# Performance work log

Hardware: AMD Instinct MI355X
Metric: run time of the kernel (lower is better)

Reference implementation:

```python
import jax, jax.numpy as jnp
import numpy as np

B, S, E, H, NE, TOPK = 8, 1024, 768, 12, 8, 2
F = 4 * E
DH = E // H

def _ln(x, g, b, eps=1e-5):
    m = jnp.mean(x, axis=-1, keepdims=True)
    v = jnp.mean((x - m) ** 2, axis=-1, keepdims=True)
    return (x - m) / jnp.sqrt(v + eps) * g + b

def _expert(x, lg, lb, w1, b1, w2, b2):
    # Expert: LayerNorm -> Linear(E,4E) -> GELU(exact) -> Linear(4E,E); dropout is identity in eval
    h = _ln(x, lg, lb)
    h = jax.nn.gelu(h @ w1.T + b1, approximate=False)
    return h @ w2.T + b2

def setup_inputs():
    key = jax.random.key(0)
    ks = jax.random.split(key, 16)
    rn = lambda k, shape, s=0.02: jax.random.normal(k, shape, jnp.float32) * s
    return {
        'x': jax.random.normal(ks[0], (B, S, E), jnp.float32),
        'modality_type': jax.random.randint(ks[1], (B, S), 0, 2).astype(jnp.int32),
        'norm1_g': jnp.ones((E,), jnp.float32), 'norm1_b': jnp.zeros((E,), jnp.float32),
        'norm2_g': jnp.ones((E,), jnp.float32), 'norm2_b': jnp.zeros((E,), jnp.float32),
        'in_proj_w': rn(ks[2], (3 * E, E)), 'in_proj_b': jnp.zeros((3 * E,), jnp.float32),
        'out_proj_w': rn(ks[3], (E, E)), 'out_proj_b': jnp.zeros((E,), jnp.float32),
        'router_w': rn(ks[4], (NE, E)), 'router_b': jnp.zeros((NE,), jnp.float32),
        'spec_ln_g': jnp.ones((3, E), jnp.float32), 'spec_ln_b': jnp.zeros((3, E), jnp.float32),
        'spec_w1': rn(ks[5], (3, F, E)), 'spec_b1': jnp.zeros((3, F), jnp.float32),
        'spec_w2': rn(ks[6], (3, E, F)), 'spec_b2': jnp.zeros((3, E), jnp.float32),
        'gen_ln_g': jnp.ones((NE, E), jnp.float32), 'gen_ln_b': jnp.zeros((NE, E), jnp.float32),
        'gen_w1': rn(ks[7], (NE, F, E)), 'gen_b1': jnp.zeros((NE, F), jnp.float32),
        'gen_w2': rn(ks[8], (NE, E, F)), 'gen_b2': jnp.zeros((NE, E), jnp.float32),
    }

def _forward(x, modality_type, norm1_g, norm1_b, norm2_g, norm2_b, in_proj_w, in_proj_b,
             out_proj_w, out_proj_b, router_w, router_b,
             spec_ln_g, spec_ln_b, spec_w1, spec_b1, spec_w2, spec_b2,
             gen_ln_g, gen_ln_b, gen_w1, gen_b1, gen_w2, gen_b2):
    # --- self-attention block (pre-norm + residual), matches nn.MultiheadAttention ---
    residual = x
    xn = _ln(x, norm1_g, norm1_b)
    qkv = xn @ in_proj_w.T + in_proj_b                          # [B,S,3E]
    q, k, v = jnp.split(qkv, 3, axis=-1)
    q = q.reshape(B, S, H, DH); k = k.reshape(B, S, H, DH); v = v.reshape(B, S, H, DH)
    scores = jnp.einsum('bqhd,bkhd->bhqk', q, k) / jnp.sqrt(jnp.float32(DH))
    attn = jax.nn.softmax(scores, axis=-1)
    ctx = jnp.einsum('bhqk,bkhd->bqhd', attn, v).reshape(B, S, E)
    x = residual + (ctx @ out_proj_w.T + out_proj_b)

    # --- MoE block (pre-norm + residual) ---
    residual = x
    xn = _ln(x, norm2_g, norm2_b)
    expert_out = _expert(xn, spec_ln_g[0], spec_ln_b[0], spec_w1[0], spec_b1[0], spec_w2[0], spec_b2[0])
    # modality experts: vision on tokens with type==0, text on type==1 (not a fusion layer)
    vmask = (modality_type == 0).astype(xn.dtype)[..., None]
    tmask = (modality_type == 1).astype(xn.dtype)[..., None]
    expert_out = expert_out + vmask * _expert(xn, spec_ln_g[1], spec_ln_b[1], spec_w1[1], spec_b1[1], spec_w2[1], spec_b2[1])
    expert_out = expert_out + tmask * _expert(xn, spec_ln_g[2], spec_ln_b[2], spec_w1[2], spec_b1[2], spec_w2[2], spec_b2[2])

    # --- router: softmax -> top_k -> renormalize over top_k ---
    logits = xn @ router_w.T + router_b                         # [B,S,NE]
    probs = jax.nn.softmax(logits, axis=-1)
    topk_probs, topk_idx = jax.lax.top_k(probs, TOPK)
    topk_w = jax.nn.softmax(topk_probs, axis=-1)                # [B,S,TOPK]

    # --- dispatch/combine: per-expert combine coefficient; experts are per-token so
    # dense masked compute is mathematically identical to the torch gather/scatter loop ---
    for e in range(NE):
        coef = jnp.sum(topk_w * (topk_idx == e), axis=-1)[..., None]   # [B,S,1]
        expert_out = expert_out + coef * _expert(xn, gen_ln_g[e], gen_ln_b[e], gen_w1[e], gen_b1[e], gen_w2[e], gen_b2[e])

    return residual + expert_out

def reference(x, modality_type, norm1_g, norm1_b, norm2_g, norm2_b, in_proj_w, in_proj_b,
              out_proj_w, out_proj_b, router_w, router_b,
              spec_ln_g, spec_ln_b, spec_w1, spec_b1, spec_w2, spec_b2,
              gen_ln_g, gen_ln_b, gen_w1, gen_b1, gen_w2, gen_b2):
    return _forward(x, modality_type, norm1_g, norm1_b, norm2_g, norm2_b, in_proj_w, in_proj_b,
                    out_proj_w, out_proj_b, router_w, router_b,
                    spec_ln_g, spec_ln_b, spec_w1, spec_b1, spec_w2, spec_b2,
                    gen_ln_g, gen_ln_b, gen_w1, gen_b1, gen_w2, gen_b2)
```

## Files before the change

kernel.cpp:

```cpp
#include <hip/hip_runtime.h>
#include <cstdint>

#define NTOK 8192
#define EDIM 768
#define FDIM 3072

using bf16x8 = __attribute__((ext_vector_type(8))) __bf16;
using f32x4  = __attribute__((ext_vector_type(4))) float;

__device__ __forceinline__ float b2f(ushort u){ union{uint32_t i; float f;} v; v.i = ((uint32_t)u)<<16; return v.f; }
__device__ __forceinline__ ushort f2b(float f){ union{float f; uint32_t i;} v; v.f=f; uint32_t r = v.i + 0x7fffu + ((v.i>>16)&1u); return (ushort)(r>>16); }
__device__ __forceinline__ float gelu_f(float v){
  float c = v*(1.5957691216f + 0.0713548162726f*v*v);
  return v / (1.f + __expf(-c));
}
__device__ __forceinline__ void gload16(const ushort* g, ushort* l){
  __builtin_amdgcn_global_load_lds((const __attribute__((address_space(1))) void*)g,
                                   (__attribute__((address_space(3))) void*)l, 16, 0, 0);
}

__global__ __launch_bounds__(256) void conv_w(const float* w0,const float* w1,const float* w2,
                                              const float* w3,const float* w4,const float* w5,
                                              const float* slg, const float* glg,
                                              ushort* pool)
{
  size_t idx4 = (size_t)blockIdx.x*256 + threadIdx.x;
  size_t e = idx4*4;
  const float* src; size_t base; int region;
  if      (e <  1769472u){src=w0;base=0;        region=0;}
  else if (e <  2359296u){src=w1;base=1769472u; region=1;}
  else if (e <  9437184u){src=w2;base=2359296u; region=2;}
  else if (e < 16515072u){src=w3;base=9437184u; region=3;}
  else if (e < 35389440u){src=w4;base=16515072u;region=4;}
  else                   {src=w5;base=35389440u;region=5;}
  size_t within = e - base;
  f32x4 f = *(const f32x4*)(src + within);
  if (region==2){
    int ex = (int)(within/2359296u); int col = (int)(within%768u);
    f32x4 g = *(const f32x4*)(slg + ex*768 + col);
    f[0]*=g[0]; f[1]*=g[1]; f[2]*=g[2]; f[3]*=g[3];
  } else if (region==4){
    int ex = (int)(within/2359296u); int col = (int)(within%768u);
    f32x4 g = *(const f32x4*)(glg + ex*768 + col);
    f[0]*=g[0]; f[1]*=g[1]; f[2]*=g[2]; f[3]*=g[3];
  }
  ushort4 u; u.x=f2b(f[0]); u.y=f2b(f[1]); u.z=f2b(f[2]); u.w=f2b(f[3]);
  *(ushort4*)(pool+e) = u;
}

__global__ __launch_bounds__(256) void b1fold_k(const float* __restrict__ sw1, const float* __restrict__ gw1,
                                                const float* __restrict__ sb1, const float* __restrict__ gb1,
                                                const float* __restrict__ slb, const float* __restrict__ glb,
                                                float* __restrict__ b1p)
{
  int j = blockIdx.x*4 + (threadIdx.x>>6);
  int lane = threadIdx.x & 63;
  int je = j / FDIM, f = j % FDIM;
  const float* wrow = (je<3) ? sw1 + ((size_t)je*FDIM + f)*EDIM : gw1 + ((size_t)(je-3)*FDIM + f)*EDIM;
  const float* lb   = (je<3) ? slb + (size_t)je*EDIM : glb + (size_t)(je-3)*EDIM;
  float s = 0.f;
  #pragma unroll
  for (int i=0;i<12;i++){ int d = lane + 64*i; s += wrow[d]*lb[d]; }
  #pragma unroll
  for (int o=32;o>0;o>>=1) s += __shfl_xor(s,o);
  if (lane==0){
    float base = (je<3) ? sb1[je*FDIM+f] : gb1[(je-3)*FDIM+f];
    b1p[j] = base + s;
  }
}

__global__ __launch_bounds__(256) void out_init(const float* __restrict__ x, const float* __restrict__ bo,
                                                float* __restrict__ out)
{
  size_t i = ((size_t)blockIdx.x*256 + threadIdx.x)*4;
  int col = (int)(i % EDIM);
  f32x4 xv = *(const f32x4*)(x+i);
  f32x4 bv = *(const f32x4*)(bo+col);
  f32x4 r = { xv[0]+bv[0], xv[1]+bv[1], xv[2]+bv[2], xv[3]+bv[3] };
  *(f32x4*)(out+i) = r;
}

__global__ __launch_bounds__(256) void ln1_k(const float* __restrict__ x, const float* __restrict__ g,
                                             const float* __restrict__ b, ushort* __restrict__ out)
{
  int w = blockIdx.x*4 + (threadIdx.x>>6);
  int lane = threadIdx.x & 63;
  const float* xr = x + (size_t)w*EDIM;
  float v[12]; float s=0.f, s2=0.f;
  #pragma unroll
  for (int i=0;i<12;i++){ v[i]=xr[lane+64*i]; s+=v[i]; s2+=v[i]*v[i]; }
  #pragma unroll
  for (int o=32;o>0;o>>=1){ s += __shfl_xor(s,o); s2 += __shfl_xor(s2,o); }
  float mu = s*(1.f/768.f);
  float rs = rsqrtf(s2*(1.f/768.f) - mu*mu + 1e-5f);
  ushort* op = out + (size_t)w*EDIM;
  #pragma unroll
  for (int i=0;i<12;i++){ int d=lane+64*i; op[d] = f2b((v[i]-mu)*rs*g[d] + b[d]); }
}

__global__ __launch_bounds__(256) void lnr_k(const float* __restrict__ x1, const float* __restrict__ g2,
                                             const float* __restrict__ b2, const float* __restrict__ rw,
                                             const float* __restrict__ rbv,
                                             ushort* __restrict__ z, float* __restrict__ coef)
{
  int w = blockIdx.x*4 + (threadIdx.x>>6);
  int lane = threadIdx.x & 63;
  const float* xr = x1 + (size_t)w*EDIM;
  float v[12]; float s=0.f, s2=0.f;
  #pragma unroll
  for (int i=0;i<12;i++){ v[i]=xr[lane+64*i]; s+=v[i]; s2+=v[i]*v[i]; }
  #pragma unroll
  for (int o=32;o>0;o>>=1){ s += __shfl_xor(s,o); s2 += __shfl_xor(s2,o); }
  float mu = s*(1.f/768.f);
  float rs = rsqrtf(s2*(1.f/768.f) - mu*mu + 1e-5f);
  float xn[12]; s=0.f; s2=0.f;
  #pragma unroll
  for (int i=0;i<12;i++){ int d=lane+64*i; xn[i]=(v[i]-mu)*rs*g2[d]+b2[d]; s+=xn[i]; s2+=xn[i]*xn[i]; }
  float pl[8] = {0.f,0.f,0.f,0.f,0.f,0.f,0.f,0.f};
  #pragma unroll
  for (int i=0;i<12;i++){
    int d=lane+64*i; float xv=xn[i];
    #pragma unroll
    for (int e=0;e<8;e++) pl[e] += xv * rw[e*EDIM + d];
  }
  #pragma unroll
  for (int o=32;o>0;o>>=1){ s += __shfl_xor(s,o); s2 += __shfl_xor(s2,o); }
  float mu2 = s*(1.f/768.f);
  float rs2 = rsqrtf(s2*(1.f/768.f) - mu2*mu2 + 1e-5f);
  ushort* op = z + (size_t)w*EDIM;
  #pragma unroll
  for (int i=0;i<12;i++){ int d=lane+64*i; op[d] = f2b((xn[i]-mu2)*rs2); }
  #pragma unroll
  for (int e=0;e<8;e++){
    #pragma unroll
    for (int o=32;o>0;o>>=1) pl[e] += __shfl_xor(pl[e], o);
  }
  float lgt[8]; float mx = -1e30f;
  #pragma unroll
  for (int e=0;e<8;e++){ lgt[e]=pl[e]+rbv[e]; mx = fmaxf(mx, lgt[e]); }
  float p[8]; float den=0.f;
  #pragma unroll
  for (int e=0;e<8;e++){ p[e]=__expf(lgt[e]-mx); den+=p[e]; }
  float inv = 1.f/den;
  #pragma unroll
  for (int e=0;e<8;e++) p[e]*=inv;
  int i1=0;
  #pragma unroll
  for (int e=1;e<8;e++) if (p[e]>p[i1]) i1=e;
  int i2=(i1==0)?1:0;
  #pragma unroll
  for (int e=0;e<8;e++){ if (e==i1) continue; if (p[e]>p[i2]) i2=e; }
  float w1 = 1.f/(1.f+__expf(p[i2]-p[i1]));
  float w2 = 1.f - w1;
  if (lane < 8){
    float c = (lane==i1)? w1 : ((lane==i2)? w2 : 0.f);
    coef[(size_t)w*8 + lane] = c;
  }
}

__global__ __launch_bounds__(256) void build_lists(const int* __restrict__ mt, const float* __restrict__ coef,
                                                   ushort* __restrict__ lists, ushort* __restrict__ inv,
                                                   int* __restrict__ cnt)
{
  const int job = blockIdx.x;
  ushort* list = lists + (size_t)job*NTOK;
  __shared__ int wsum[4];
  int base = 0;
  const int lane = threadIdx.x & 63, wv = threadIdx.x >> 6;
  for (int c0=0; c0<NTOK; c0+=256){
    int t = c0 + threadIdx.x;
    bool flag;
    if (job==0)      flag = (mt[t]==0);
    else if (job==1) flag = (mt[t]==1);
    else             flag = (coef[(size_t)t*8 + (job-2)] != 0.0f);
    unsigned long long bal = __ballot(flag);
    int pre = __popcll(bal & ((1ull<<lane)-1ull));
    if (lane==0) wsum[wv] = __popcll(bal);
    __syncthreads();
    int off = base + pre;
    for (int k=0;k<wv;k++) off += wsum[k];
    int tot = wsum[0]+wsum[1]+wsum[2]+wsum[3];
    if (flag){ list[off] = (ushort)t; inv[(size_t)job*NTOK + t] = (ushort)off; }
    base += tot;
    __syncthreads();
  }
  if (threadIdx.x==0){ cnt[job+1] = base; if (job==0) cnt[0] = NTOK; }
}

__global__ __launch_bounds__(256) void gather_k(const float* __restrict__ coef, const int* __restrict__ mt,
                                                const ushort* __restrict__ inv, const int* __restrict__ cnt,
                                                const ushort* __restrict__ outC, float* __restrict__ out,
                                                int phase)
{
  int t = blockIdx.x*4 + (threadIdx.x>>6);
  int lane = threadIdx.x & 63;
  int r0, r1; float c0=1.f, c1=1.f;
  if (phase==0){
    r0 = t;
    int m = mt[t];
    r1 = NTOK + (m ? cnt[1] : 0) + (int)inv[(size_t)m*NTOK + t];
  } else {
    int found=0; int rr[2]={0,0}; float cc[2]={0.f,0.f}; int base=0;
    #pragma unroll
    for (int e=0;e<8;e++){
      float ce = coef[(size_t)t*8+e];
      if (ce != 0.f && found<2){ rr[found]=base+(int)inv[(size_t)(2+e)*NTOK + t]; cc[found]=ce; found++; }
      base += cnt[3+e];
    }
    r0=rr[0]; r1=rr[1]; c0=cc[0]; c1=cc[1];
  }
  const ushort* pa = outC + (size_t)r0*EDIM;
  const ushort* pb = outC + (size_t)r1*EDIM;
  float* po = out + (size_t)t*EDIM;
  #pragma unroll
  for (int i=0;i<3;i++){
    int d = lane*4 + 256*i;
    ushort4 ua = *(const ushort4*)(pa+d);
    ushort4 ub = *(const ushort4*)(pb+d);
    f32x4 o = *(f32x4*)(po+d);
    o[0] += c0*b2f(ua.x) + c1*b2f(ub.x);
    o[1] += c0*b2f(ua.y) + c1*b2f(ub.y);
    o[2] += c0*b2f(ua.z) + c1*b2f(ub.z);
    o[3] += c0*b2f(ua.w) + c1*b2f(ub.w);
    *(f32x4*)(po+d) = o;
  }
}

struct GemmArgs {
  const ushort* A; const ushort* B;
  const float* bias;
  ushort* outBF;
  int K, ldc;
};

__global__ __launch_bounds__(256) void gemm_k(GemmArgs g)
{
  const int mb = blockIdx.x, nb = blockIdx.y;
  __shared__ __align__(1024) ushort As[128*32];
  __shared__ __align__(1024) ushort Bs[128*32];
  const int tid = threadIdx.x;
  const int lane = tid & 63, w = tid >> 6;
  const int seg = lane & 3;
  const int lrow = w*16 + (lane>>2);
  const int p = (lane>>3)&3;
  ushort* ldsA0 = As + (size_t)w*512;
  ushort* ldsA1 = As + (size_t)(w+4)*512;
  ushort* ldsB0 = Bs + (size_t)w*512;
  ushort* ldsB1 = Bs + (size_t)(w+4)*512;
  const int KK = g.K;
  const ushort* pA0 = g.A + (size_t)(mb*128 + lrow)*KK + (seg^p)*8;
  const ushort* pA1 = pA0 + (size_t)64*KK;
  const ushort* pB0 = g.B + (size_t)(nb*128 + lrow)*KK + (seg^p)*8;
  const ushort* pB1 = pB0 + (size_t)64*KK;
  const int nst = KK >> 5;
  f32x4 acc[4][4];
  #pragma unroll
  for (int m=0;m<4;m++)
    #pragma unroll
    for (int n=0;n<4;n++) acc[m][n] = (f32x4){0.f,0.f,0.f,0.f};
  const int fr = lane & 15, fq = lane >> 4;
  const int pr = (fr>>1)&3;
  const int so = (fq^pr)*8;
  const int rb_ = (w>>1)*64, cb_ = (w&1)*64;
  for (int kt=0; kt<nst; ++kt){
    __syncthreads();
    gload16(pA0, ldsA0); gload16(pA1, ldsA1);
    gload16(pB0, ldsB0); gload16(pB1, ldsB1);
    pA0 += 32; pA1 += 32; pB0 += 32; pB1 += 32;
    __syncthreads();
    bf16x8 af[4], bfr[4];
    #pragma unroll
    for (int m=0;m<4;m++) af[m]  = *(const bf16x8*)&As[(rb_ + m*16 + fr)*32 + so];
    #pragma unroll
    for (int n=0;n<4;n++) bfr[n] = *(const bf16x8*)&Bs[(cb_ + n*16 + fr)*32 + so];
    #pragma unroll
    for (int m=0;m<4;m++)
      #pragma unroll
      for (int n=0;n<4;n++)
        acc[m][n] = __builtin_amdgcn_mfma_f32_16x16x32_bf16(af[m], bfr[n], acc[m][n], 0, 0, 0);
  }
  #pragma unroll
  for (int m=0;m<4;m++){
    #pragma unroll
    for (int j=0;j<4;j++){
      const int row = mb*128 + rb_ + m*16 + fq*4 + j;
      #pragma unroll
      for (int n=0;n<4;n++){
        const int col = nb*128 + cb_ + n*16 + fr;
        g.outBF[(size_t)row*g.ldc + col] = f2b(acc[m][n][j] + g.bias[col]);
      }
    }
  }
}

struct FArgs {
  const ushort* z; ushort* hidden; const ushort* ctx; const ushort* wo;
  float* out; ushort* outC;
  const ushort* lists; const ushort* inv; const int* cnt; const float* coef;
  const ushort* sw1; const ushort* gw1; const ushort* sw2; const ushort* gw2;
  const float* b1p; const float* sb2; const float* gb2;
  int jobBase; int compact; int mode;
};

__device__ __forceinline__ size_t job_hoff(const FArgs& a, int job){
  size_t h = 0;
  if (a.compact){
    if (job==1) h = NTOK;
    else if (job==2) h = NTOK + (size_t)a.cnt[1];
    else if (job>=3){ for (int k=3;k<job;k++) h += (size_t)a.cnt[k]; }
  }
  return h;
}

__global__ __launch_bounds__(512) void ffn1_k(FArgs a)
{
  const int job = a.jobBase + blockIdx.z;
  const int cntj = (job==0) ? NTOK : a.cnt[job];
  const int mb = blockIdx.x, nb = blockIdx.y;
  if (mb*128 >= cntj) return;
  const ushort* list = (job==0) ? nullptr : a.lists + (size_t)(job-1)*NTOK;
  const ushort* B = (job<3) ? a.sw1+(size_t)job*FDIM*EDIM : a.gw1+(size_t)(job-3)*FDIM*EDIM;
  const float* bias = a.b1p + (size_t)job*FDIM;
  const size_t hoff = job_hoff(a, job);
  __shared__ __align__(1024) ushort As[128*32];
  __shared__ __align__(1024) ushort Bs[256*32];
  const int tid = threadIdx.x;
  const int lane = tid & 63, w = tid >> 6;
  const int seg = lane & 3;
  const int lrow = w*16 + (lane>>2);
  const int p = (lane>>3)&3;
  ushort* ldsA  = As + (size_t)w*512;
  ushort* ldsB0 = Bs + (size_t)w*512;
  ushort* ldsB1 = Bs + (size_t)(w+8)*512;
  const int r0 = mb*128 + lrow;
  const int tA = list ? (int)list[min(r0,cntj-1)] : min(r0,cntj-1);
  const ushort* pA  = a.z + (size_t)tA*EDIM + (seg^p)*8;
  const ushort* pB0 = B + (size_t)(nb*256 + lrow)*EDIM + (seg^p)*8;
  const ushort* pB1 = pB0 + (size_t)128*EDIM;
  f32x4 acc[4][4];
  #pragma unroll
  for (int m=0;m<4;m++)
    #pragma unroll
    for (int n=0;n<4;n++) acc[m][n] = (f32x4){0.f,0.f,0.f,0.f};
  const int fr = lane & 15, fq = lane >> 4;
  const int pr = (fr>>1)&3;
  const int so = (fq^pr)*8;
  const int rb_ = (w>>2)*64;
  const int cb_ = (w&3)*64;
  for (int kt=0; kt<24; ++kt){
    __syncthreads();
    gload16(pA, ldsA);
    gload16(pB0, ldsB0); gload16(pB1, ldsB1);
    pA += 32; pB0 += 32; pB1 += 32;
    __syncthreads();
    bf16x8 af[4], bfr[4];
    #pragma unroll
    for (int m=0;m<4;m++) af[m]  = *(const bf16x8*)&As[(rb_ + m*16 + fr)*32 + so];
    #pragma unroll
    for (int n=0;n<4;n++) bfr[n] = *(const bf16x8*)&Bs[(cb_ + n*16 + fr)*32 + so];
    #pragma unroll
    for (int m=0;m<4;m++)
      #pragma unroll
      for (int n=0;n<4;n++)
        acc[m][n] = __builtin_amdgcn_mfma_f32_16x16x32_bf16(af[m], bfr[n], acc[m][n], 0, 0, 0);
  }
  #pragma unroll
  for (int m=0;m<4;m++){
    #pragma unroll
    for (int j=0;j<4;j++){
      const int row = mb*128 + rb_ + m*16 + fq*4 + j;
      if (row < cntj){
        #pragma unroll
        for (int n=0;n<4;n++){
          const int col = nb*256 + cb_ + n*16 + fr;
          a.hidden[(hoff+row)*FDIM + col] = f2b(gelu_f(acc[m][n][j] + bias[col]));
        }
      }
    }
  }
}

__global__ __launch_bounds__(256) void ffn2_k(FArgs a)
{
  const bool op = (a.jobBase < 0);
  const int job = op ? -1 : a.jobBase + blockIdx.z;
  const int cntj = op ? NTOK : ((job==0) ? NTOK : a.cnt[job]);
  const int mb = blockIdx.x, nb = blockIdx.y;
  if (mb*64 >= cntj) return;
  const ushort* list = (op || job==0) ? nullptr : a.lists + (size_t)(job-1)*NTOK;
  const ushort* Abase; int lda; const ushort* B; const float* bias = nullptr;
  const float* coefp = nullptr; int eidx = 0;
  if (op){ Abase = a.ctx; lda = EDIM; B = a.wo; }
  else {
    lda = FDIM;
    Abase = a.hidden + job_hoff(a, job)*FDIM;
    if (job<3){ B=a.sw2+(size_t)job*(size_t)EDIM*FDIM; bias=a.sb2+(size_t)job*EDIM; }
    else { eidx=job-3; B=a.gw2+(size_t)eidx*(size_t)EDIM*FDIM; bias=a.gb2+(size_t)eidx*EDIM; coefp=a.coef; }
  }
  const size_t hoff = op ? 0 : job_hoff(a, job);
  const int nst = lda >> 5;
  __shared__ __align__(1024) ushort As[64*32];
  __shared__ __align__(1024) ushort Bs[128*32];
  const int tid = threadIdx.x;
  const int lane = tid & 63, w = tid >> 6;
  const int seg = lane & 3;
  const int lrow = w*16 + (lane>>2);
  const int p = (lane>>3)&3;
  ushort* ldsA  = As + (size_t)w*512;
  ushort* ldsB0 = Bs + (size_t)w*512;
  ushort* ldsB1 = Bs + (size_t)(w+4)*512;
  const int r0 = mb*64 + lrow;
  const ushort* pA  = Abase + (size_t)min(r0,cntj-1)*lda + (seg^p)*8;
  const ushort* pB0 = B + (size_t)(nb*128 + lrow)*lda + (seg^p)*8;
  const ushort* pB1 = pB0 + (size_t)64*lda;
  f32x4 acc[4][2];
  #pragma unroll
  for (int m=0;m<4;m++)
    #pragma unroll
    for (int n=0;n<2;n++) acc[m][n] = (f32x4){0.f,0.f,0.f,0.f};
  const int fr = lane & 15, fq = lane >> 4;
  const int pr = (fr>>1)&3;
  const int so = (fq^pr)*8;
  const int cb_ = w*32;
  for (int kt=0; kt<nst; ++kt){
    __syncthreads();
    gload16(pA, ldsA);
    gload16(pB0, ldsB0); gload16(pB1, ldsB1);
    pA += 32; pB0 += 32; pB1 += 32;
    __syncthreads();
    bf16x8 af[4], bfr[2];
    #pragma unroll
    for (int m=0;m<4;m++) af[m]  = *(const bf16x8*)&As[(m*16 + fr)*32 + so];
    #pragma unroll
    for (int n=0;n<2;n++) bfr[n] = *(const bf16x8*)&Bs[(cb_ + n*16 + fr)*32 + so];
    #pragma unroll
    for (int m=0;m<4;m++)
      #pragma unroll
      for (int n=0;n<2;n++)
        acc[m][n] = __builtin_amdgcn_mfma_f32_16x16x32_bf16(af[m], bfr[n], acc[m][n], 0, 0, 0);
  }
  #pragma unroll
  for (int m=0;m<4;m++){
    #pragma unroll
    for (int j=0;j<4;j++){
      const int row = mb*64 + m*16 + fq*4 + j;
      if (row < cntj){
        #pragma unroll
        for (int n=0;n<2;n++){
          const int col = nb*128 + cb_ + n*16 + fr;
          float v = acc[m][n][j];
          if (op){
            a.out[(size_t)row*EDIM + col] += v;
          } else if (a.mode==1){
            a.outC[(hoff+row)*EDIM + col] = f2b(v + bias[col]);
          } else {
            const int tok = list ? (int)list[row] : row;
            const float c = coefp ? coefp[(size_t)tok*8 + eidx] : 1.0f;
            atomicAdd(&a.out[(size_t)tok*EDIM + col], c*(v + bias[col]));
          }
        }
      }
    }
  }
}

__global__ __launch_bounds__(256) void attn_k(const ushort* __restrict__ qkv, ushort* __restrict__ ctx)
{
  const int qb = blockIdx.x, bh = blockIdx.y;
  const int b = bh/12, h = bh%12;
  const int tid = threadIdx.x;
  const int lane = tid & 63, w = tid >> 6;
  const int fr = lane & 15, fq = lane >> 4;
  __shared__ __align__(16) ushort Ks[4096];
  __shared__ __align__(16) ushort Vts[4096];
  __shared__ __align__(16) ushort Ps[4096];
  const size_t tokq = (size_t)b*1024 + (size_t)qb*64;

  bf16x8 qf[2];
  {
    const ushort* qp = qkv + (tokq + w*16 + fr)*2304 + h*64 + fq*8;
    qf[0] = *(const bf16x8*)(qp);
    qf[1] = *(const bf16x8*)(qp + 32);
  }
  f32x4 o[4];
  #pragma unroll
  for (int nt=0;nt<4;nt++) o[nt] = (f32x4){0.f,0.f,0.f,0.f};
  float m[4] = {-1e30f,-1e30f,-1e30f,-1e30f};
  float l[4] = {0.f,0.f,0.f,0.f};

  const int skr = tid>>3, skc = (tid&7)*8;
  const int svd = (tid&15)*4, svk = (tid>>4)*4;

  for (int kt=0; kt<16; ++kt){
    __syncthreads();
    const size_t tokk = (size_t)b*1024 + (size_t)kt*64;
    #pragma unroll
    for (int pp=0;pp<2;pp++){
      int row = skr + pp*32;
      uint4 kq = *(const uint4*)(qkv + (tokk+row)*2304 + 768 + h*64 + skc);
      *(uint4*)&Ks[row*64 + (skc ^ ((row&7)<<3))] = kq;
    }
    {
      union { ushort4 v4[4]; ushort s[16]; } tv;
      #pragma unroll
      for (int i=0;i<4;i++)
        tv.v4[i] = *(const ushort4*)(qkv + (tokk+svk+i)*2304 + 1536 + h*64 + svd);
      #pragma unroll
      for (int j=0;j<4;j++){
        ushort4 tj; tj.x=tv.s[j]; tj.y=tv.s[4+j]; tj.z=tv.s[8+j]; tj.w=tv.s[12+j];
        int dr = svd + j;
        *(ushort4*)&Vts[dr*64 + (svk ^ ((dr&7)<<3))] = tj;
      }
    }
    __syncthreads();
    f32x4 s[4];
    #pragma unroll
    for (int nt=0;nt<4;nt++){
      s[nt] = (f32x4){0.f,0.f,0.f,0.f};
      int kr = nt*16 + fr;
      const ushort* kb = &Ks[kr*64];
      int sw = (kr&7)<<3;
      bf16x8 k0 = *(const bf16x8*)&kb[(fq*8) ^ sw];
      bf16x8 k1 = *(const bf16x8*)&kb[(fq*8+32) ^ sw];
      s[nt] = __builtin_amdgcn_mfma_f32_16x16x32_bf16(qf[0], k0, s[nt], 0,0,0);
      s[nt] = __builtin_amdgcn_mfma_f32_16x16x32_bf16(qf[1], k1, s[nt], 0,0,0);
    }
    float a_[4], pr[4][4];
    #pragma unroll
    for (int j=0;j<4;j++){
      float mx = fmaxf(fmaxf(s[0][j],s[1][j]), fmaxf(s[2][j],s[3][j])) * 0.125f;
      mx = fmaxf(mx, __shfl_xor(mx,1));
      mx = fmaxf(mx, __shfl_xor(mx,2));
      mx = fmaxf(mx, __shfl_xor(mx,4));
      mx = fmaxf(mx, __shfl_xor(mx,8));
      float mn = fmaxf(m[j], mx);
      float aa = __expf(m[j] - mn);
      m[j] = mn; a_[j] = aa;
      float ss = 0.f;
      #pragma unroll
      for (int nt=0;nt<4;nt++){
        float pv = __expf(s[nt][j]*0.125f - mn);
        pr[nt][j] = pv; ss += pv;
      }
      ss += __shfl_xor(ss,1);
      ss += __shfl_xor(ss,2);
      ss += __shfl_xor(ss,4);
      ss += __shfl_xor(ss,8);
      l[j] = l[j]*aa + ss;
    }
    #pragma unroll
    for (int nt=0;nt<4;nt++){
      #pragma unroll
      for (int j=0;j<4;j++){
        int row = fq*4 + j;
        Ps[w*1024 + row*64 + ((nt*16+fr) ^ ((row&7)<<3))] = f2b(pr[nt][j]);
        o[nt][j] *= a_[j];
      }
    }
    #pragma unroll
    for (int ks=0; ks<2; ++ks){
      int kvo = ks*32 + fq*8;
      bf16x8 pf = *(const bf16x8*)&Ps[w*1024 + fr*64 + (kvo ^ ((fr&7)<<3))];
      #pragma unroll
      for (int nt=0;nt<4;nt++){
        int dr = nt*16 + fr;
        bf16x8 vf = *(const bf16x8*)&Vts[dr*64 + (kvo ^ ((dr&7)<<3))];
        o[nt] = __builtin_amdgcn_mfma_f32_16x16x32_bf16(pf, vf, o[nt], 0,0,0);
      }
    }
  }
  float inv[4];
  #pragma unroll
  for (int j=0;j<4;j++) inv[j] = 1.f/l[j];
  ushort* cp = ctx + (tokq + w*16)*768 + h*64;
  #pragma unroll
  for (int nt=0;nt<4;nt++){
    #pragma unroll
    for (int j=0;j<4;j++){
      cp[(size_t)(fq*4+j)*768 + nt*16 + fr] = f2b(o[nt][j]*inv[j]);
    }
  }
}

#define OFF_POOL   0u
#define OFF_Z      108527616u
#define OFF_COEF   121110528u
#define OFF_LISTS  121372672u
#define OFF_INV    121536512u
#define OFF_CNT    121700352u
#define OFF_B1P    121700608u
#define OFF_QKV    121835776u
#define OFF_CTX    159584512u
#define OFF_XN1    172167424u
#define WS_GROUPED 222499072u
#define OFF_OUTC   222499072u
#define WS_BIG     247664896u

extern "C" void kernel_launch(void* const* d_in, const int* in_sizes, int n_in,
                              void* d_out, int out_size, void* d_ws, size_t ws_size,
                              hipStream_t stream)
{
  const float* x    = (const float*)d_in[0];
  const int*   mt   = (const int*)d_in[1];
  const float* n1g  = (const float*)d_in[2];
  const float* n1b  = (const float*)d_in[3];
  const float* n2g  = (const float*)d_in[4];
  const float* n2b  = (const float*)d_in[5];
  const float* wqkv = (const float*)d_in[6];
  const float* bqkv = (const float*)d_in[7];
  const float* wo   = (const float*)d_in[8];
  const float* bo   = (const float*)d_in[9];
  const float* rw   = (const float*)d_in[10];
  const float* rb   = (const float*)d_in[11];
  const float* slg  = (const float*)d_in[12];
  const float* slb  = (const float*)d_in[13];
  const float* sw1  = (const float*)d_in[14];
  const float* sb1  = (const float*)d_in[15];
  const float* sw2  = (const float*)d_in[16];
  const float* sb2  = (const float*)d_in[17];
  const float* glg  = (const float*)d_in[18];
  const float* glb  = (const float*)d_in[19];
  const float* gw1  = (const float*)d_in[20];
  const float* gb1  = (const float*)d_in[21];
  const float* gw2  = (const float*)d_in[22];
  const float* gb2  = (const float*)d_in[23];
  float* out = (float*)d_out;
  char* ws = (char*)d_ws;

  ushort* pool  = (ushort*)(ws + OFF_POOL);
  ushort* z     = (ushort*)(ws + OFF_Z);
  float*  coef  = (float*) (ws + OFF_COEF);
  ushort* lists = (ushort*)(ws + OFF_LISTS);
  ushort* invp  = (ushort*)(ws + OFF_INV);
  int*    cnt   = (int*)   (ws + OFF_CNT);
  float*  b1p   = (float*) (ws + OFF_B1P);
  ushort* qkv   = (ushort*)(ws + OFF_QKV);
  ushort* ctx   = (ushort*)(ws + OFF_CTX);
  ushort* xn1   = (ushort*)(ws + OFF_XN1);
  ushort* hidden= (ushort*)(ws + OFF_QKV);
  ushort* outC  = (ushort*)(ws + OFF_OUTC);

  ushort* pWqkv = pool + 0;
  ushort* pWo   = pool + 1769472;
  ushort* pSw1  = pool + 2359296;
  ushort* pSw2  = pool + 9437184;
  ushort* pGw1  = pool + 16515072;
  ushort* pGw2  = pool + 35389440;

  const int tier = (ws_size >= (size_t)WS_BIG) ? 2 : ((ws_size >= (size_t)WS_GROUPED) ? 1 : 0);

  conv_w<<<52992, 256, 0, stream>>>(wqkv, wo, sw1, sw2, gw1, gw2, slg, glg, pool);
  b1fold_k<<<8448, 256, 0, stream>>>(sw1, gw1, sb1, gb1, slb, glb, b1p);
  ln1_k<<<2048, 256, 0, stream>>>(x, n1g, n1b, xn1);
  { GemmArgs a{}; a.A=xn1; a.B=pWqkv; a.bias=bqkv; a.outBF=qkv; a.K=768; a.ldc=2304;
    gemm_k<<<dim3(64,18),256,0,stream>>>(a); }
  attn_k<<<dim3(16,96),256,0,stream>>>(qkv, ctx);
  out_init<<<6144,256,0,stream>>>(x, bo, out);

  FArgs fa{};
  fa.z=z; fa.hidden=hidden; fa.ctx=ctx; fa.wo=pWo; fa.out=out; fa.outC=outC;
  fa.lists=lists; fa.inv=invp; fa.cnt=cnt; fa.coef=coef;
  fa.sw1=pSw1; fa.gw1=pGw1; fa.sw2=pSw2; fa.gw2=pGw2;
  fa.b1p=b1p; fa.sb2=sb2; fa.gb2=gb2;

  { FArgs a = fa; a.jobBase = -1; a.compact = 0; a.mode = 0;
    ffn2_k<<<dim3(128,6,1),256,0,stream>>>(a); }

  lnr_k<<<2048,256,0,stream>>>(out, n2g, n2b, rw, rb, z, coef);
  build_lists<<<10,256,0,stream>>>(mt, coef, lists, invp, cnt);

  if (tier==2){
    { FArgs a = fa; a.jobBase = 0; a.compact = 1; a.mode = 1;
      ffn1_k<<<dim3(64,12,3),512,0,stream>>>(a);
      ffn2_k<<<dim3(128,6,3),256,0,stream>>>(a); }
    gather_k<<<2048,256,0,stream>>>(coef, mt, invp, cnt, outC, out, 0);
    { FArgs a = fa; a.jobBase = 3; a.compact = 1; a.mode = 1;
      ffn1_k<<<dim3(64,12,8),512,0,stream>>>(a);
      ffn2_k<<<dim3(128,6,8),256,0,stream>>>(a); }
    gather_k<<<2048,256,0,stream>>>(coef, mt, invp, cnt, outC, out, 1);
  } else if (tier==1){
    { FArgs a = fa; a.jobBase = 0; a.compact = 1; a.mode = 0;
      ffn1_k<<<dim3(64,12,3),512,0,stream>>>(a);
      ffn2_k<<<dim3(128,6,3),256,0,stream>>>(a); }
    { FArgs a = fa; a.jobBase = 3; a.compact = 1; a.mode = 0;
      ffn1_k<<<dim3(64,12,8),512,0,stream>>>(a);
      ffn2_k<<<dim3(128,6,8),256,0,stream>>>(a); }
  } else {
    for (int j=0;j<11;j++){
      FArgs a = fa; a.jobBase = j; a.compact = 0; a.mode = 0;
      ffn1_k<<<dim3(64,12,1),512,0,stream>>>(a);
      ffn2_k<<<dim3(128,6,1),256,0,stream>>>(a);
    }
  }
}
```

Measured before the change: 1.083 ms.

## Double-buffer LDS tiles with async global loads in all GEMM kernels

Splits the shared-memory A/B tiles of gemm_k, ffn1_k and ffn2_k into two buffers. The next K-slice is fetched with global_load_lds while the current one feeds the MFMAs. The two __syncthreads per step become hand-written s_waitcnt vmcnt(N) plus s_barrier, so the wait covers only the older stage's loads. This doubles LDS use per block, which may lower occupancy. gemm_k now hardcodes 24 K-steps, which assumes K=768.

```diff
diff --git a/kernel.cpp b/kernel.cpp
--- a/kernel.cpp
+++ b/kernel.cpp
@@ -18,6 +18,10 @@
   __builtin_amdgcn_global_load_lds((const __attribute__((address_space(1))) void*)g,
                                    (__attribute__((address_space(3))) void*)l, 16, 0, 0);
 }
+__device__ __forceinline__ void vbar3(){ asm volatile("s_waitcnt vmcnt(3)\ns_barrier" ::: "memory"); }
+__device__ __forceinline__ void vbar4(){ asm volatile("s_waitcnt vmcnt(4)\ns_barrier" ::: "memory"); }
+__device__ __forceinline__ void vbar0(){ asm volatile("s_waitcnt vmcnt(0)\ns_barrier" ::: "memory"); }
+__device__ __forceinline__ void barX(){  asm volatile("s_barrier" ::: "memory"); }
 
 __global__ __launch_bounds__(256) void conv_w(const float* w0,const float* w1,const float* w2,
                                               const float* w3,const float* w4,const float* w5,
@@ -236,23 +240,21 @@
 __global__ __launch_bounds__(256) void gemm_k(GemmArgs g)
 {
   const int mb = blockIdx.x, nb = blockIdx.y;
-  __shared__ __align__(1024) ushort As[128*32];
-  __shared__ __align__(1024) ushort Bs[128*32];
+  __shared__ __align__(1024) ushort As0[128*32];
+  __shared__ __align__(1024) ushort As1[128*32];
+  __shared__ __align__(1024) ushort Bs0[128*32];
+  __shared__ __align__(1024) ushort Bs1[128*32];
   const int tid = threadIdx.x;
   const int lane = tid & 63, w = tid >> 6;
   const int seg = lane & 3;
   const int lrow = w*16 + (lane>>2);
   const int p = (lane>>3)&3;
-  ushort* ldsA0 = As + (size_t)w*512;
-  ushort* ldsA1 = As + (size_t)(w+4)*512;
-  ushort* ldsB0 = Bs + (size_t)w*512;
-  ushort* ldsB1 = Bs + (size_t)(w+4)*512;
+  const int dA0 = w*512, dA1 = (w+4)*512;
   const int KK = g.K;
   const ushort* pA0 = g.A + (size_t)(mb*128 + lrow)*KK + (seg^p)*8;
   const ushort* pA1 = pA0 + (size_t)64*KK;
   const ushort* pB0 = g.B + (size_t)(nb*128 + lrow)*KK + (seg^p)*8;
   const ushort* pB1 = pB0 + (size_t)64*KK;
-  const int nst = KK >> 5;
   f32x4 acc[4][4];
   #pragma unroll
   for (int m=0;m<4;m++)
@@ -262,22 +264,32 @@
   const int pr = (fr>>1)&3;
   const int so = (fq^pr)*8;
   const int rb_ = (w>>1)*64, cb_ = (w&1)*64;
-  for (int kt=0; kt<nst; ++kt){
-    __syncthreads();
-    gload16(pA0, ldsA0); gload16(pA1, ldsA1);
-    gload16(pB0, ldsB0); gload16(pB1, ldsB1);
+
+  auto stage = [&](ushort* AS, ushort* BS){
+    gload16(pA0, AS+dA0); gload16(pA1, AS+dA1);
+    gload16(pB0, BS+dA0); gload16(pB1, BS+dA1);
     pA0 += 32; pA1 += 32; pB0 += 32; pB1 += 32;
-    __syncthreads();
+  };
+  auto comp = [&](const ushort* AS, const ushort* BS){
     bf16x8 af[4], bfr[4];
     #pragma unroll
-    for (int m=0;m<4;m++) af[m]  = *(const bf16x8*)&As[(rb_ + m*16 + fr)*32 + so];
-    #pragma unroll
-    for (int n=0;n<4;n++) bfr[n] = *(const bf16x8*)&Bs[(cb_ + n*16 + fr)*32 + so];
+    for (int m=0;m<4;m++) af[m]  = *(const bf16x8*)&AS[(rb_ + m*16 + fr)*32 + so];
+    #pragma unroll
+    for (int n=0;n<4;n++) bfr[n] = *(const bf16x8*)&BS[(cb_ + n*16 + fr)*32 + so];
     #pragma unroll
     for (int m=0;m<4;m++)
       #pragma unroll
       for (int n=0;n<4;n++)
         acc[m][n] = __builtin_amdgcn_mfma_f32_16x16x32_bf16(af[m], bfr[n], acc[m][n], 0, 0, 0);
+  };
+
+  stage(As0,Bs0);
+  for (int kt=0; kt<24; kt+=2){
+    stage(As1,Bs1); vbar4();
+    comp(As0,Bs0);  barX();
+    if (kt+2<24){ stage(As0,Bs0); vbar4(); }
+    else        { vbar0(); }
+    comp(As1,Bs1);  barX();
   }
   #pragma unroll
   for (int m=0;m<4;m++){
@@ -322,16 +334,16 @@
   const ushort* B = (job<3) ? a.sw1+(size_t)job*FDIM*EDIM : a.gw1+(size_t)(job-3)*FDIM*EDIM;
   const float* bias = a.b1p + (size_t)job*FDIM;
   const size_t hoff = job_hoff(a, job);
-  __shared__ __align__(1024) ushort As[128*32];
-  __shared__ __align__(1024) ushort Bs[256*32];
+  __shared__ __align__(1024) ushort As0[128*32];
+  __shared__ __align__(1024) ushort As1[128*32];
+  __shared__ __align__(1024) ushort Bs0[256*32];
+  __shared__ __align__(1024) ushort Bs1[256*32];
   const int tid = threadIdx.x;
   const int lane = tid & 63, w = tid >> 6;
   const int seg = lane & 3;
   const int lrow = w*16 + (lane>>2);
   const int p = (lane>>3)&3;
-  ushort* ldsA  = As + (size_t)w*512;
-  ushort* ldsB0 = Bs + (size_t)w*512;
-  ushort* ldsB1 = Bs + (size_t)(w+8)*512;
+  const int dA = w*512, dB0 = w*512, dB1 = (w+8)*512;
   const int r0 = mb*128 + lrow;
   const int tA = list ? (int)list[min(r0,cntj-1)] : min(r0,cntj-1);
   const ushort* pA  = a.z + (size_t)tA*EDIM + (seg^p)*8;
@@ -347,22 +359,32 @@
   const int so = (fq^pr)*8;
   const int rb_ = (w>>2)*64;
   const int cb_ = (w&3)*64;
-  for (int kt=0; kt<24; ++kt){
-    __syncthreads();
-    gload16(pA, ldsA);
-    gload16(pB0, ldsB0); gload16(pB1, ldsB1);
+
+  auto stage = [&](ushort* AS, ushort* BS){
+    gload16(pA, AS+dA);
+    gload16(pB0, BS+dB0); gload16(pB1, BS+dB1);
     pA += 32; pB0 += 32; pB1 += 32;
-    __syncthreads();
+  };
+  auto comp = [&](const ushort* AS, const ushort* BS){
     bf16x8 af[4], bfr[4];
     #pragma unroll
-    for (int m=0;m<4;m++) af[m]  = *(const bf16x8*)&As[(rb_ + m*16 + fr)*32 + so];
-    #pragma unroll
-    for (int n=0;n<4;n++) bfr[n] = *(const bf16x8*)&Bs[(cb_ + n*16 + fr)*32 + so];
+    for (int m=0;m<4;m++) af[m]  = *(const bf16x8*)&AS[(rb_ + m*16 + fr)*32 + so];
+    #pragma unroll
+    for (int n=0;n<4;n++) bfr[n] = *(const bf16x8*)&BS[(cb_ + n*16 + fr)*32 + so];
     #pragma unroll
     for (int m=0;m<4;m++)
       #pragma unroll
       for (int n=0;n<4;n++)
         acc[m][n] = __builtin_amdgcn_mfma_f32_16x16x32_bf16(af[m], bfr[n], acc[m][n], 0, 0, 0);
+  };
+
+  stage(As0,Bs0);
+  for (int kt=0; kt<24; kt+=2){
+    stage(As1,Bs1); vbar3();
+    comp(As0,Bs0);  barX();
+    if (kt+2<24){ stage(As0,Bs0); vbar3(); }
+    else        { vbar0(); }
+    comp(As1,Bs1);  barX();
   }
   #pragma unroll
   for (int m=0;m<4;m++){
@@ -399,16 +421,16 @@
   }
   const size_t hoff = op ? 0 : job_hoff(a, job);
   const int nst = lda >> 5;
-  __shared__ __align__(1024) ushort As[64*32];
-  __shared__ __align__(1024) ushort Bs[128*32];
+  __shared__ __align__(1024) ushort As0[64*32];
+  __shared__ __align__(1024) ushort As1[64*32];
+  __shared__ __align__(1024) ushort Bs0[128*32];
+  __shared__ __align__(1024) ushort Bs1[128*32];
   const int tid = threadIdx.x;
   const int lane = tid & 63, w = tid >> 6;
   const int seg = lane & 3;
   const int lrow = w*16 + (lane>>2);
   const int p = (lane>>3)&3;
-  ushort* ldsA  = As + (size_t)w*512;
-  ushort* ldsB0 = Bs + (size_t)w*512;
-  ushort* ldsB1 = Bs + (size_t)(w+4)*512;
+  const int dA = w*512, dB0 = w*512, dB1 = (w+4)*512;
   const int r0 = mb*64 + lrow;
   const ushort* pA  = Abase + (size_t)min(r0,cntj-1)*lda + (seg^p)*8;
   const ushort* pB0 = B + (size_t)(nb*128 + lrow)*lda + (seg^p)*8;
@@ -422,22 +444,32 @@
   const int pr = (fr>>1)&3;
   const int so = (fq^pr)*8;
   const int cb_ = w*32;
-  for (int kt=0; kt<nst; ++kt){
-    __syncthreads();
-    gload16(pA, ldsA);
-    gload16(pB0, ldsB0); gload16(pB1, ldsB1);
+
+  auto stage = [&](ushort* AS, ushort* BS){
+    gload16(pA, AS+dA);
+    gload16(pB0, BS+dB0); gload16(pB1, BS+dB1);
     pA += 32; pB0 += 32; pB1 += 32;
-    __syncthreads();
+  };
+  auto comp = [&](const ushort* AS, const ushort* BS){
     bf16x8 af[4], bfr[2];
     #pragma unroll
-    for (int m=0;m<4;m++) af[m]  = *(const bf16x8*)&As[(m*16 + fr)*32 + so];
-    #pragma unroll
-    for (int n=0;n<2;n++) bfr[n] = *(const bf16x8*)&Bs[(cb_ + n*16 + fr)*32 + so];
+    for (int m=0;m<4;m++) af[m]  = *(const bf16x8*)&AS[(m*16 + fr)*32 + so];
+    #pragma unroll
+    for (int n=0;n<2;n++) bfr[n] = *(const bf16x8*)&BS[(cb_ + n*16 + fr)*32 + so];
     #pragma unroll
     for (int m=0;m<4;m++)
       #pragma unroll
       for (int n=0;n<2;n++)
         acc[m][n] = __builtin_amdgcn_mfma_f32_16x16x32_bf16(af[m], bfr[n], acc[m][n], 0, 0, 0);
+  };
+
+  stage(As0,Bs0);
+  for (int kt=0; kt<nst; kt+=2){
+    stage(As1,Bs1); vbar3();
+    comp(As0,Bs0);  barX();
+    if (kt+2<nst){ stage(As0,Bs0); vbar3(); }
+    else         { vbar0(); }
+    comp(As1,Bs1);  barX();
   }
   #pragma unroll
   for (int m=0;m<4;m++){
```

Result: slower. 1.173 ms (+8.3%).
